# Kernel tuning notes

Hardware: AMD Instinct MI355X
Metric: run time of the kernel (lower is better)

## Reference

```python
import jax, jax.numpy as jnp
import numpy as np

B, V, K, CL1_F = 8192, 1000, 5, 5
HID, OUT, NLAYERS = 256, 10, 4
BN_EPS = 1e-5


def _make_laplacian(rng):
    A = (rng.random((V, V)) < 0.01).astype(np.float32)
    A = np.triu(A, 1)
    A = A + A.T
    d = np.maximum(A.sum(1), 1.0)
    dinv = 1.0 / np.sqrt(d)
    Lap = np.eye(V, dtype=np.float32) - (dinv[:, None] * A * dinv[None, :])
    lmax = float(np.linalg.eigvalsh(Lap.astype(np.float64))[-1])
    return Lap.astype(np.float32), np.array([lmax], dtype=np.float32)


def setup_inputs() -> dict:
    key = jax.random.key(0)
    ks = jax.random.split(key, 16)
    rng = np.random.default_rng(0)
    Lap, lmax = _make_laplacian(rng)
    s = lambda fan_in: 1.0 / np.sqrt(fan_in)
    inp = {
        "x": jax.random.normal(ks[0], (B, V), dtype=jnp.float32),
        "L": jnp.asarray(Lap),
        "lmax": jnp.asarray(lmax),
        "cl1_W": jax.random.uniform(ks[1], (CL1_F, K), jnp.float32, -s(K), s(K)),
        "cl1_b": jax.random.uniform(ks[2], (CL1_F,), jnp.float32, -s(K), s(K)),
        "fc1_W": jax.random.uniform(ks[3], (HID, 625), jnp.float32, -s(625), s(625)),
        "fc1_b": jax.random.uniform(ks[4], (HID,), jnp.float32, -s(625), s(625)),
        "bn_gamma": jnp.ones((NLAYERS, HID), jnp.float32),
        "bn_beta": jnp.zeros((NLAYERS, HID), jnp.float32),
        "bn_mean": 0.1 * jax.random.normal(ks[5], (NLAYERS, HID), dtype=jnp.float32),
        "bn_var": jnp.ones((NLAYERS, HID), jnp.float32) + 0.1 * jax.random.uniform(ks[6], (NLAYERS, HID), dtype=jnp.float32),
        "lin1_W": jax.random.uniform(ks[7], (HID, HID), jnp.float32, -s(HID), s(HID)),
        "lin1_b": jax.random.uniform(ks[8], (HID,), jnp.float32, -s(HID), s(HID)),
        "lin2_W": jax.random.uniform(ks[9], (OUT, HID), jnp.float32, -s(HID), s(HID)),
        "lin2_b": jax.random.uniform(ks[10], (OUT,), jnp.float32, -s(HID), s(HID)),
    }
    return inp


def reference(x, L, lmax, cl1_W, cl1_b, fc1_W, fc1_b,
              bn_gamma, bn_beta, bn_mean, bn_var,
              lin1_W, lin1_b, lin2_W, lin2_b):
    # ---- graph_conv_cheby (Fin = 1) ----
    Lr = 2.0 * L / lmax[0] - jnp.eye(V, dtype=L.dtype)  # rescale_L
    x0 = x.T                              # [V, B]  (Fin*B with Fin=1)
    x1 = Lr @ x0
    basis = [x0, x1]
    for _ in range(2, K):                 # Chebyshev recursion T_k = 2 L T_{k-1} - T_{k-2}
        basis.append(2.0 * (Lr @ basis[-1]) - basis[-2])
    xk = jnp.stack(basis, 0)              # [K, V, B]
    feat = xk.transpose(2, 1, 0).reshape(B * V, K)       # [B*V, Fin*K]
    h = feat @ cl1_W.T + cl1_b            # cl1: Linear(5,5)
    h = jax.nn.relu(h.reshape(B, V, CL1_F))
    # ---- graph_max_pool p=8 over node dim ----
    h = h.reshape(B, V // 8, 8, CL1_F).max(axis=2)       # [B, 125, 5]
    h = h.reshape(B, 625)
    h = h @ fc1_W.T + fc1_b               # [B, 256]
    # ---- per-layer BN (eval) + ReLU (dropout inactive in eval); convs never applied ----
    xs = []
    for i in range(NLAYERS):
        h = (h - bn_mean[i]) * (bn_gamma[i] / jnp.sqrt(bn_var[i] + BN_EPS)) + bn_beta[i]
        h = jax.nn.relu(h)
        xs.append(h)
    # ---- JumpingKnowledge (max) ----
    z = jnp.max(jnp.stack(xs, 0), axis=0)
    z = jax.nn.relu(z @ lin1_W.T + lin1_b)
    out = z @ lin2_W.T + lin2_b
    return jax.nn.log_softmax(out, axis=-1)
```

## Files before the change

### kernel.cpp

```cpp
#include <hip/hip_runtime.h>

typedef unsigned int u32;
typedef unsigned short u16;
typedef unsigned long long u64;

typedef __attribute__((ext_vector_type(8))) short s8v;
typedef __attribute__((ext_vector_type(4))) float f4v;
typedef __attribute__((ext_vector_type(8))) _Float16 h8v;

#define B_SZ   8192
#define V_SZ   1000
#define KCH    5
#define MAXDEG 32

__device__ __forceinline__ u16 f2bf(float f) {
    u32 u = __float_as_uint(f);
    u32 r = (u + 0x7FFFu + ((u >> 16) & 1u)) >> 16;
    return (u16)r;
}
__device__ __forceinline__ float bf2f(u16 h) { return __uint_as_float(((u32)h) << 16); }

__device__ __forceinline__ float fmix_lo(float acc, float w, u32 h2) {
    asm("v_fma_mix_f32 %0, %1, %2, %0 op_sel_hi:[0,1,0]"
        : "+v"(acc) : "v"(w), "v"(h2));
    return acc;
}
__device__ __forceinline__ float fmix_hi(float acc, float w, u32 h2) {
    asm("v_fma_mix_f32 %0, %1, %2, %0 op_sel:[0,1,0] op_sel_hi:[0,1,0]"
        : "+v"(acc) : "v"(w), "v"(h2));
    return acc;
}

__global__ __launch_bounds__(256) void k_prep(const float* __restrict__ L,
                                              const float* __restrict__ lmax,
                                              float* __restrict__ wts,
                                              u16* __restrict__ colsu,
                                              int* __restrict__ cnts,
                                              float* __restrict__ diagw,
                                              const float* __restrict__ fc1W,
                                              const float* __restrict__ lin1W,
                                              const float* __restrict__ gam,
                                              const float* __restrict__ bet,
                                              const float* __restrict__ mea,
                                              const float* __restrict__ var,
                                              u16* __restrict__ fc1w_b,
                                              u16* __restrict__ lin1w_b,
                                              float* __restrict__ bn_a,
                                              float* __restrict__ bn_c) {
    if (blockIdx.x < 250) {
        int wid  = threadIdx.x >> 6;
        int lane = threadIdx.x & 63;
        int row  = blockIdx.x * 4 + wid;
        if (row >= V_SZ) return;
        float s = 2.0f / lmax[0];
        const float* Lrow = L + (u64)row * V_SZ;
        int cnt = 0;
        for (int c0 = 0; c0 < V_SZ; c0 += 64) {
            int c = c0 + lane;
            float val = 0.0f;
            if (c < V_SZ && c != row) val = Lrow[c];
            bool nz = (val != 0.0f);
            u64 m = __ballot(nz);
            int pos = cnt + __popcll(m & ((1ull << lane) - 1ull));
            if (nz && pos < MAXDEG) {
                int idx = ((pos >> 2) * V_SZ + row) * 4 + (pos & 3);
                wts[idx]   = val * s;
                colsu[idx] = (u16)c;
            }
            cnt += __popcll(m);
        }
        int cc = cnt < MAXDEG ? cnt : MAXDEG;
        for (int e = cc + lane; e < MAXDEG; e += 64) {
            int idx = ((e >> 2) * V_SZ + row) * 4 + (e & 3);
            wts[idx]   = 0.0f;
            colsu[idx] = 0;
        }
        if (lane == 0) {
            cnts[row]  = cc;
            diagw[row] = s * Lrow[row] - 1.0f;
        }
    } else {
        int t = (blockIdx.x - 250) * 256 + threadIdx.x;
        if (t < 256 * 640) {
            int r = t / 640, c = t - r * 640;
            fc1w_b[t] = (c < 625) ? f2bf(fc1W[r * 625 + c]) : (u16)0;
        }
        if (t < 256 * 256) lin1w_b[t] = f2bf(lin1W[t]);
        if (t < 4 * 256) {
            float a = gam[t] * rsqrtf(var[t] + 1e-5f);
            bn_a[t] = a;
            bn_c[t] = bet[t] - mea[t] * a;
        }
    }
}

__global__ __launch_bounds__(1024) void k_cheby(const float* __restrict__ x,
                                                const float4* __restrict__ wts4,
                                                const uint2* __restrict__ cols2,
                                                const int* __restrict__ cnts,
                                                const float* __restrict__ diagw,
                                                const float* __restrict__ cl1W,
                                                const float* __restrict__ cl1b,
                                                u16* __restrict__ pooled) {
    __shared__ __align__(16) h8v hbuf[2][V_SZ];
    __shared__ float cws[25];
    __shared__ float cbs[5];
    int t  = threadIdx.x;
    int b0 = blockIdx.x * 8;

    if (t < 25) cws[t] = cl1W[t];
    if (t < 5)  cbs[t] = cl1b[t];

    const bool own = (t < V_SZ);
    const int  tc  = own ? t : (V_SZ - 1);

    float d0 = own ? diagw[tc] : 0.0f;
    int   n0 = own ? ((cnts[tc] + 3) >> 2) : 0;

    float4 pm1l = make_float4(0.f, 0.f, 0.f, 0.f), pm1h = pm1l, pm2l, pm2h;
    if (own) {
        pm1l.x = x[(u64)(b0 + 0) * V_SZ + t];
        pm1l.y = x[(u64)(b0 + 1) * V_SZ + t];
        pm1l.z = x[(u64)(b0 + 2) * V_SZ + t];
        pm1l.w = x[(u64)(b0 + 3) * V_SZ + t];
        pm1h.x = x[(u64)(b0 + 4) * V_SZ + t];
        pm1h.y = x[(u64)(b0 + 5) * V_SZ + t];
        pm1h.z = x[(u64)(b0 + 6) * V_SZ + t];
        pm1h.w = x[(u64)(b0 + 7) * V_SZ + t];
        h8v hv;
        hv[0] = (_Float16)pm1l.x; hv[1] = (_Float16)pm1l.y;
        hv[2] = (_Float16)pm1l.z; hv[3] = (_Float16)pm1l.w;
        hv[4] = (_Float16)pm1h.x; hv[5] = (_Float16)pm1h.y;
        hv[6] = (_Float16)pm1h.z; hv[7] = (_Float16)pm1h.w;
        hbuf[0][t] = hv;
    }
    pm2l = pm1l; pm2h = pm1h;
    __syncthreads();

    float4 fl[5], fh[5];
#pragma unroll
    for (int f = 0; f < 5; ++f) {
        float w = cws[f * 5];
        fl[f] = make_float4(w * pm1l.x, w * pm1l.y, w * pm1l.z, w * pm1l.w);
        fh[f] = make_float4(w * pm1h.x, w * pm1h.y, w * pm1h.z, w * pm1h.w);
    }

#pragma unroll
    for (int k = 1; k < KCH; ++k) {
        const uint4* prevb = (const uint4*)hbuf[(k - 1) & 1];
        h8v*         curb  = hbuf[k & 1];

        if (own) {
            float4 al = make_float4(d0 * pm1l.x, d0 * pm1l.y, d0 * pm1l.z, d0 * pm1l.w);
            float4 ah = make_float4(d0 * pm1h.x, d0 * pm1h.y, d0 * pm1h.z, d0 * pm1h.w);
            float4 wq = wts4[tc];
            uint2  cq = cols2[tc];
            for (int q = 0; q < n0; ++q) {
                float4 wqn = wq;
                uint2  cqn = cq;
                if (q + 1 < n0) {
                    wqn = wts4[(q + 1) * V_SZ + tc];
                    cqn = cols2[(q + 1) * V_SZ + tc];
                }
                u32 c0i = cq.x & 0xFFFFu, c1i = cq.x >> 16;
                u32 c2i = cq.y & 0xFFFFu, c3i = cq.y >> 16;
                uint4 g0 = prevb[c0i];
                uint4 g1 = prevb[c1i];
                uint4 g2 = prevb[c2i];
                uint4 g3 = prevb[c3i];
                al.x = fmix_lo(al.x, wq.x, g0.x); al.y = fmix_hi(al.y, wq.x, g0.x);
                al.z = fmix_lo(al.z, wq.x, g0.y); al.w = fmix_hi(al.w, wq.x, g0.y);
                ah.x = fmix_lo(ah.x, wq.x, g0.z); ah.y = fmix_hi(ah.y, wq.x, g0.z);
                ah.z = fmix_lo(ah.z, wq.x, g0.w); ah.w = fmix_hi(ah.w, wq.x, g0.w);
                al.x = fmix_lo(al.x, wq.y, g1.x); al.y = fmix_hi(al.y, wq.y, g1.x);
                al.z = fmix_lo(al.z, wq.y, g1.y); al.w = fmix_hi(al.w, wq.y, g1.y);
                ah.x = fmix_lo(ah.x, wq.y, g1.z); ah.y = fmix_hi(ah.y, wq.y, g1.z);
                ah.z = fmix_lo(ah.z, wq.y, g1.w); ah.w = fmix_hi(ah.w, wq.y, g1.w);
                al.x = fmix_lo(al.x, wq.z, g2.x); al.y = fmix_hi(al.y, wq.z, g2.x);
                al.z = fmix_lo(al.z, wq.z, g2.y); al.w = fmix_hi(al.w, wq.z, g2.y);
                ah.x = fmix_lo(ah.x, wq.z, g2.z); ah.y = fmix_hi(ah.y, wq.z, g2.z);
                ah.z = fmix_lo(ah.z, wq.z, g2.w); ah.w = fmix_hi(ah.w, wq.z, g2.w);
                al.x = fmix_lo(al.x, wq.w, g3.x); al.y = fmix_hi(al.y, wq.w, g3.x);
                al.z = fmix_lo(al.z, wq.w, g3.y); al.w = fmix_hi(al.w, wq.w, g3.y);
                ah.x = fmix_lo(ah.x, wq.w, g3.z); ah.y = fmix_hi(ah.y, wq.w, g3.z);
                ah.z = fmix_lo(ah.z, wq.w, g3.w); ah.w = fmix_hi(ah.w, wq.w, g3.w);
                wq = wqn; cq = cqn;
            }
            if (k >= 2) {
                al.x = fmaf(2.0f, al.x, -pm2l.x); al.y = fmaf(2.0f, al.y, -pm2l.y);
                al.z = fmaf(2.0f, al.z, -pm2l.z); al.w = fmaf(2.0f, al.w, -pm2l.w);
                ah.x = fmaf(2.0f, ah.x, -pm2h.x); ah.y = fmaf(2.0f, ah.y, -pm2h.y);
                ah.z = fmaf(2.0f, ah.z, -pm2h.z); ah.w = fmaf(2.0f, ah.w, -pm2h.w);
            }
            h8v hv;
            hv[0] = (_Float16)al.x; hv[1] = (_Float16)al.y;
            hv[2] = (_Float16)al.z; hv[3] = (_Float16)al.w;
            hv[4] = (_Float16)ah.x; hv[5] = (_Float16)ah.y;
            hv[6] = (_Float16)ah.z; hv[7] = (_Float16)ah.w;
            curb[t] = hv;
            pm2l = pm1l; pm2h = pm1h;
            pm1l = al;   pm1h = ah;
#pragma unroll
            for (int f = 0; f < 5; ++f) {
                float w = cws[f * 5 + k];
                fl[f].x = fmaf(w, al.x, fl[f].x); fl[f].y = fmaf(w, al.y, fl[f].y);
                fl[f].z = fmaf(w, al.z, fl[f].z); fl[f].w = fmaf(w, al.w, fl[f].w);
                fh[f].x = fmaf(w, ah.x, fh[f].x); fh[f].y = fmaf(w, ah.y, fh[f].y);
                fh[f].z = fmaf(w, ah.z, fh[f].z); fh[f].w = fmaf(w, ah.w, fh[f].w);
            }
        }
        __syncthreads();
    }

#pragma unroll
    for (int f = 0; f < 5; ++f) {
#pragma unroll
        for (int b = 0; b < 8; ++b) {
            float c0 = (b == 0) ? fl[f].x : (b == 1) ? fl[f].y
                     : (b == 2) ? fl[f].z : (b == 3) ? fl[f].w
                     : (b == 4) ? fh[f].x : (b == 5) ? fh[f].y
                     : (b == 6) ? fh[f].z : fh[f].w;
            float s = own ? fmaxf(c0 + cbs[f], 0.0f) : 0.0f;
            s = fmaxf(s, __shfl_xor(s, 1));
            s = fmaxf(s, __shfl_xor(s, 2));
            s = fmaxf(s, __shfl_xor(s, 4));
            if ((t & 7) == 0 && own)
                pooled[(u64)(b0 + b) * 640 + (t >> 3) * 5 + f] = f2bf(s);
        }
    }
    if (t < 120) {
        int b = t / 15, c = 625 + (t % 15);
        pooled[(u64)(b0 + b) * 640 + c] = 0;
    }
}

__global__ __launch_bounds__(256) void k_tail(const u16* __restrict__ A,
                                              const u16* __restrict__ W0,
                                              const float* __restrict__ b0v,
                                              const float* __restrict__ bn_a,
                                              const float* __restrict__ bn_c,
                                              const u16* __restrict__ W1,
                                              const float* __restrict__ b1v,
                                              const float* __restrict__ W2,
                                              const float* __restrict__ b2v,
                                              float* __restrict__ out) {
    __shared__ u16   As[64][72];
    __shared__ u16   Bs[256][72];
    __shared__ u16   zs[64][264];
    __shared__ float w2s[2560];
    __shared__ float b2s[10];
    int t    = threadIdx.x;
    int lane = t & 63;
    int wid  = t >> 6;
    int r0   = blockIdx.x * 64;

    for (int c = t; c < 2560; c += 256) w2s[c] = W2[c];
    if (t < 10) b2s[t] = b2v[t];

    f4v acc[16];
#pragma unroll
    for (int j = 0; j < 16; ++j) acc[j] = (f4v){0.f, 0.f, 0.f, 0.f};

    for (int k0 = 0; k0 < 640; k0 += 64) {
        int4 ra[2], rb[8];
#pragma unroll
        for (int i = 0; i < 2; ++i) {
            int c = t + i * 256, row = c >> 3, kc = c & 7;
            ra[i] = *(const int4*)(A + (u64)(r0 + row) * 640 + k0 + kc * 8);
        }
#pragma unroll
        for (int i = 0; i < 8; ++i) {
            int c = t + i * 256, row = c >> 3, kc = c & 7;
            rb[i] = *(const int4*)(W0 + (u64)row * 640 + k0 + kc * 8);
        }
        __syncthreads();
#pragma unroll
        for (int i = 0; i < 2; ++i) {
            int c = t + i * 256, row = c >> 3, kc = c & 7;
            *(int4*)(&As[row][kc * 8]) = ra[i];
        }
#pragma unroll
        for (int i = 0; i < 8; ++i) {
            int c = t + i * 256, row = c >> 3, kc = c & 7;
            *(int4*)(&Bs[row][kc * 8]) = rb[i];
        }
        __syncthreads();
#pragma unroll
        for (int ks = 0; ks < 2; ++ks) {
            int kq = ks * 32 + (lane >> 4) * 8;
            s8v af = *(const s8v*)(&As[wid * 16 + (lane & 15)][kq]);
#pragma unroll
            for (int nt = 0; nt < 16; ++nt) {
                s8v bf = *(const s8v*)(&Bs[nt * 16 + (lane & 15)][kq]);
                acc[nt] = __builtin_amdgcn_mfma_f32_16x16x32_bf16(af, bf, acc[nt], 0, 0, 0);
            }
        }
    }
#pragma unroll
    for (int nt = 0; nt < 16; ++nt) {
        int col = nt * 16 + (lane & 15);
        float bv = b0v[col];
        float a_[4], c_[4];
#pragma unroll
        for (int i = 0; i < 4; ++i) {
            a_[i] = bn_a[i * 256 + col];
            c_[i] = bn_c[i * 256 + col];
        }
        int rb_ = wid * 16 + (lane >> 4) * 4;
#pragma unroll
        for (int r = 0; r < 4; ++r) {
            float h = acc[nt][r] + bv, z = 0.0f;
#pragma unroll
            for (int i = 0; i < 4; ++i) {
                h = fmaxf(fmaf(a_[i], h, c_[i]), 0.0f);
                z = fmaxf(z, h);
            }
            zs[rb_ + r][col] = f2bf(z);
        }
    }
    __syncthreads();

#pragma unroll
    for (int j = 0; j < 16; ++j) acc[j] = (f4v){0.f, 0.f, 0.f, 0.f};
    for (int k0 = 0; k0 < 256; k0 += 64) {
        int4 rb[8];
#pragma unroll
        for (int i = 0; i < 8; ++i) {
            int c = t + i * 256, row = c >> 3, kc = c & 7;
            rb[i] = *(const int4*)(W1 + (u64)row * 256 + k0 + kc * 8);
        }
        __syncthreads();
#pragma unroll
        for (int i = 0; i < 8; ++i) {
            int c = t + i * 256, row = c >> 3, kc = c & 7;
            *(int4*)(&Bs[row][kc * 8]) = rb[i];
        }
        __syncthreads();
#pragma unroll
        for (int ks = 0; ks < 2; ++ks) {
            int kqr = ks * 32 + (lane >> 4) * 8;
            s8v af = *(const s8v*)(&zs[wid * 16 + (lane & 15)][k0 + kqr]);
#pragma unroll
            for (int nt = 0; nt < 16; ++nt) {
                s8v bf = *(const s8v*)(&Bs[nt * 16 + (lane & 15)][kqr]);
                acc[nt] = __builtin_amdgcn_mfma_f32_16x16x32_bf16(af, bf, acc[nt], 0, 0, 0);
            }
        }
    }
#pragma unroll
    for (int nt = 0; nt < 16; ++nt) {
        int col = nt * 16 + (lane & 15);
        float bv = b1v[col];
        int rb_ = wid * 16 + (lane >> 4) * 4;
#pragma unroll
        for (int r = 0; r < 4; ++r)
            zs[rb_ + r][col] = f2bf(fmaxf(acc[nt][r] + bv, 0.0f));
    }
    __syncthreads();

    {
        int row = t >> 2, sub = t & 3;
        float a10[10];
#pragma unroll
        for (int o = 0; o < 10; ++o) a10[o] = 0.0f;
        const u32* zrow = (const u32*)(&zs[row][0]);
        for (int kk = sub * 32; kk < sub * 32 + 32; ++kk) {
            u32 pz = zrow[kk];
            float z0 = bf2f((u16)(pz & 0xFFFFu));
            float z1 = bf2f((u16)(pz >> 16));
#pragma unroll
            for (int o = 0; o < 10; ++o) {
                a10[o] = fmaf(z0, w2s[o * 256 + kk * 2], a10[o]);
                a10[o] = fmaf(z1, w2s[o * 256 + kk * 2 + 1], a10[o]);
            }
        }
#pragma unroll
        for (int o = 0; o < 10; ++o) {
            a10[o] += __shfl_xor(a10[o], 1);
            a10[o] += __shfl_xor(a10[o], 2);
        }
        if (sub == 0) {
            float l[10], mx = -1e30f;
#pragma unroll
            for (int o = 0; o < 10; ++o) { l[o] = a10[o] + b2s[o]; mx = fmaxf(mx, l[o]); }
            float s = 0.0f;
#pragma unroll
            for (int o = 0; o < 10; ++o) s += expf(l[o] - mx);
            float ls = logf(s);
            float* orow = out + (u64)(r0 + row) * 10;
#pragma unroll
            for (int o = 0; o < 10; ++o) orow[o] = l[o] - mx - ls;
        }
    }
}

extern "C" void kernel_launch(void* const* d_in, const int* in_sizes, int n_in,
                              void* d_out, int out_size, void* d_ws, size_t ws_size,
                              hipStream_t stream) {
    const float* x    = (const float*)d_in[0];
    const float* L    = (const float*)d_in[1];
    const float* lmax = (const float*)d_in[2];
    const float* cl1W = (const float*)d_in[3];
    const float* cl1b = (const float*)d_in[4];
    const float* fc1W = (const float*)d_in[5];
    const float* fc1b = (const float*)d_in[6];
    const float* gam  = (const float*)d_in[7];
    const float* bet  = (const float*)d_in[8];
    const float* mea  = (const float*)d_in[9];
    const float* var  = (const float*)d_in[10];
    const float* l1W  = (const float*)d_in[11];
    const float* l1b  = (const float*)d_in[12];
    const float* l2W  = (const float*)d_in[13];
    const float* l2b  = (const float*)d_in[14];

    char* ws = (char*)d_ws;
    float* wts     = (float*)(ws + 0);
    u16*   colsu   = (u16*)(ws + 131072);
    int*   cnts    = (int*)(ws + 196608);
    float* diagw   = (float*)(ws + 200704);
    float* bn_a    = (float*)(ws + 204800);
    float* bn_c    = (float*)(ws + 208896);
    u16*   fc1w_b  = (u16*)(ws + 212992);
    u16*   lin1w_b = (u16*)(ws + 540672);
    u16*   pooled  = (u16*)(ws + 671744);
    float* outp    = (float*)d_out;

    k_prep<<<dim3(890), dim3(256), 0, stream>>>(L, lmax, wts, colsu, cnts, diagw,
                                                fc1W, l1W, gam, bet, mea, var,
                                                fc1w_b, lin1w_b, bn_a, bn_c);
    k_cheby<<<dim3(1024), dim3(1024), 0, stream>>>(x, (const float4*)wts,
                                                   (const uint2*)colsu, cnts, diagw,
                                                   cl1W, cl1b, pooled);
    k_tail<<<dim3(128), dim3(256), 0, stream>>>(pooled, fc1w_b, fc1b, bn_a, bn_c,
                                                lin1w_b, l1b, l2W, l2b, outp);
}
```

Measured before the change: 232.8 us.

## Sort graph nodes by degree per block and pool through shared memory

Each block builds a histogram of per-node neighbor-chunk counts and counting-sorts node indices so that threads in a wavefront handle nodes with similar degree. This is meant to cut divergence in the sparse Chebyshev gather loop. The max-pool epilogue now writes ReLU'd fp16 features to shared memory and takes the max over unsigned 16-bit bit patterns, which is valid because the values are non-negative. This replaces the shuffle reduction but adds several barriers and an fp16 rounding step before the bf16 conversion.

```diff
diff --git a/kernel.cpp b/kernel.cpp
--- a/kernel.cpp
+++ b/kernel.cpp
@@ -19,6 +19,9 @@
     return (u16)r;
 }
 __device__ __forceinline__ float bf2f(u16 h) { return __uint_as_float(((u32)h) << 16); }
+__device__ __forceinline__ float h2f(u16 h) {
+    _Float16 x; __builtin_memcpy(&x, &h, 2); return (float)x;
+}
 
 __device__ __forceinline__ float fmix_lo(float acc, float w, u32 h2) {
     asm("v_fma_mix_f32 %0, %1, %2, %0 op_sel_hi:[0,1,0]"
@@ -105,37 +108,57 @@
     __shared__ __align__(16) h8v hbuf[2][V_SZ];
     __shared__ float cws[25];
     __shared__ float cbs[5];
+    __shared__ int   hist[16];
+    __shared__ u16   order[V_SZ];
     int t  = threadIdx.x;
     int b0 = blockIdx.x * 8;
 
     if (t < 25) cws[t] = cl1W[t];
     if (t < 5)  cbs[t] = cl1b[t];
+    if (t < 16) hist[t] = 0;
 
     const bool own = (t < V_SZ);
-    const int  tc  = own ? t : (V_SZ - 1);
-
-    float d0 = own ? diagw[tc] : 0.0f;
-    int   n0 = own ? ((cnts[tc] + 3) >> 2) : 0;
-
+
+    int nq_t = 0;
+    if (own) nq_t = (cnts[t] + 3) >> 2;
+    __syncthreads();
+    if (own) atomicAdd(&hist[nq_t], 1);
+    if (own) {
+        h8v hv;
+        hv[0] = (_Float16)x[(u64)(b0 + 0) * V_SZ + t];
+        hv[1] = (_Float16)x[(u64)(b0 + 1) * V_SZ + t];
+        hv[2] = (_Float16)x[(u64)(b0 + 2) * V_SZ + t];
+        hv[3] = (_Float16)x[(u64)(b0 + 3) * V_SZ + t];
+        hv[4] = (_Float16)x[(u64)(b0 + 4) * V_SZ + t];
+        hv[5] = (_Float16)x[(u64)(b0 + 5) * V_SZ + t];
+        hv[6] = (_Float16)x[(u64)(b0 + 6) * V_SZ + t];
+        hv[7] = (_Float16)x[(u64)(b0 + 7) * V_SZ + t];
+        hbuf[0][t] = hv;
+    }
+    __syncthreads();
+    if (t == 0) {
+        int acc = 0;
+#pragma unroll
+        for (int i = 0; i < 16; ++i) { int h = hist[i]; hist[i] = acc; acc += h; }
+    }
+    __syncthreads();
+    if (own) {
+        int pos = atomicAdd(&hist[nq_t], 1);
+        order[pos] = (u16)t;
+    }
+    __syncthreads();
+
+    const int r  = own ? (int)order[t] : 0;
+    float d0 = 0.0f; int n0 = 0;
     float4 pm1l = make_float4(0.f, 0.f, 0.f, 0.f), pm1h = pm1l, pm2l, pm2h;
     if (own) {
-        pm1l.x = x[(u64)(b0 + 0) * V_SZ + t];
-        pm1l.y = x[(u64)(b0 + 1) * V_SZ + t];
-        pm1l.z = x[(u64)(b0 + 2) * V_SZ + t];
-        pm1l.w = x[(u64)(b0 + 3) * V_SZ + t];
-        pm1h.x = x[(u64)(b0 + 4) * V_SZ + t];
-        pm1h.y = x[(u64)(b0 + 5) * V_SZ + t];
-        pm1h.z = x[(u64)(b0 + 6) * V_SZ + t];
-        pm1h.w = x[(u64)(b0 + 7) * V_SZ + t];
-        h8v hv;
-        hv[0] = (_Float16)pm1l.x; hv[1] = (_Float16)pm1l.y;
-        hv[2] = (_Float16)pm1l.z; hv[3] = (_Float16)pm1l.w;
-        hv[4] = (_Float16)pm1h.x; hv[5] = (_Float16)pm1h.y;
-        hv[6] = (_Float16)pm1h.z; hv[7] = (_Float16)pm1h.w;
-        hbuf[0][t] = hv;
+        d0 = diagw[r];
+        n0 = (cnts[r] + 3) >> 2;
+        h8v hv0 = hbuf[0][r];
+        pm1l = make_float4((float)hv0[0], (float)hv0[1], (float)hv0[2], (float)hv0[3]);
+        pm1h = make_float4((float)hv0[4], (float)hv0[5], (float)hv0[6], (float)hv0[7]);
     }
     pm2l = pm1l; pm2h = pm1h;
-    __syncthreads();
 
     float4 fl[5], fh[5];
 #pragma unroll
@@ -153,14 +176,14 @@
         if (own) {
             float4 al = make_float4(d0 * pm1l.x, d0 * pm1l.y, d0 * pm1l.z, d0 * pm1l.w);
             float4 ah = make_float4(d0 * pm1h.x, d0 * pm1h.y, d0 * pm1h.z, d0 * pm1h.w);
-            float4 wq = wts4[tc];
-            uint2  cq = cols2[tc];
+            float4 wq = wts4[r];
+            uint2  cq = cols2[r];
             for (int q = 0; q < n0; ++q) {
                 float4 wqn = wq;
                 uint2  cqn = cq;
                 if (q + 1 < n0) {
-                    wqn = wts4[(q + 1) * V_SZ + tc];
-                    cqn = cols2[(q + 1) * V_SZ + tc];
+                    wqn = wts4[(q + 1) * V_SZ + r];
+                    cqn = cols2[(q + 1) * V_SZ + r];
                 }
                 u32 c0i = cq.x & 0xFFFFu, c1i = cq.x >> 16;
                 u32 c2i = cq.y & 0xFFFFu, c3i = cq.y >> 16;
@@ -197,7 +220,7 @@
             hv[2] = (_Float16)al.z; hv[3] = (_Float16)al.w;
             hv[4] = (_Float16)ah.x; hv[5] = (_Float16)ah.y;
             hv[6] = (_Float16)ah.z; hv[7] = (_Float16)ah.w;
-            curb[t] = hv;
+            curb[r] = hv;
             pm2l = pm1l; pm2h = pm1h;
             pm1l = al;   pm1h = ah;
 #pragma unroll
@@ -212,21 +235,32 @@
         __syncthreads();
     }
 
-#pragma unroll
     for (int f = 0; f < 5; ++f) {
-#pragma unroll
-        for (int b = 0; b < 8; ++b) {
-            float c0 = (b == 0) ? fl[f].x : (b == 1) ? fl[f].y
-                     : (b == 2) ? fl[f].z : (b == 3) ? fl[f].w
-                     : (b == 4) ? fh[f].x : (b == 5) ? fh[f].y
-                     : (b == 6) ? fh[f].z : fh[f].w;
-            float s = own ? fmaxf(c0 + cbs[f], 0.0f) : 0.0f;
-            s = fmaxf(s, __shfl_xor(s, 1));
-            s = fmaxf(s, __shfl_xor(s, 2));
-            s = fmaxf(s, __shfl_xor(s, 4));
-            if ((t & 7) == 0 && own)
-                pooled[(u64)(b0 + b) * 640 + (t >> 3) * 5 + f] = f2bf(s);
-        }
+        if (own) {
+            h8v hv;
+            hv[0] = (_Float16)fmaxf(fl[f].x + cbs[f], 0.0f);
+            hv[1] = (_Float16)fmaxf(fl[f].y + cbs[f], 0.0f);
+            hv[2] = (_Float16)fmaxf(fl[f].z + cbs[f], 0.0f);
+            hv[3] = (_Float16)fmaxf(fl[f].w + cbs[f], 0.0f);
+            hv[4] = (_Float16)fmaxf(fh[f].x + cbs[f], 0.0f);
+            hv[5] = (_Float16)fmaxf(fh[f].y + cbs[f], 0.0f);
+            hv[6] = (_Float16)fmaxf(fh[f].z + cbs[f], 0.0f);
+            hv[7] = (_Float16)fmaxf(fh[f].w + cbs[f], 0.0f);
+            hbuf[1][r] = hv;
+        }
+        __syncthreads();
+        if (own) {
+            int p = t >> 3, b = t & 7;
+            const u16* sc = (const u16*)hbuf[1];
+            u16 m = 0;
+#pragma unroll
+            for (int j = 0; j < 8; ++j) {
+                u16 v = sc[(8 * p + j) * 8 + b];
+                m = (v > m) ? v : m;
+            }
+            pooled[(u64)(b0 + b) * 640 + p * 5 + f] = f2bf(h2f(m));
+        }
+        __syncthreads();
     }
     if (t < 120) {
         int b = t / 15, c = 625 + (t % 15);
```

Measured after the change: 217.2 us. 6.7% less time.
